# Kernel tuning notes

Hardware: AMD Instinct MI355X
Metric: run time of the kernel (lower is better)

## Reference

```python
import jax, jax.numpy as jnp
import numpy as np

B, F, H, T = 32, 128, 256, 2048


def setup_inputs() -> dict:
    key = jax.random.key(0)
    ks = jax.random.split(key, 20)
    s = 0.05
    x = jax.random.normal(ks[0], (B, 1, T, F), dtype=jnp.float32)
    mask = (jax.random.uniform(ks[1], (B, 1, T, F)) < 0.5).astype(jnp.float32)
    delta = jax.random.uniform(ks[2], (B, 1, T, F), dtype=jnp.float32)  # time since last obs
    inp = jnp.concatenate([x, mask, delta], axis=1)  # [B, 3, T, F]
    p = lambda k, shape: jax.random.normal(k, shape, dtype=jnp.float32) * s
    return {
        "input": inp,
        "x_mean": p(ks[3], (F,)),
        # layer 0: input decay (diagonal), hidden decay, gates
        "w_dx": p(ks[4], (F,)), "b_dx": p(ks[5], (F,)),
        "W_dh0": p(ks[6], (F, H)), "b_dh0": p(ks[7], (H,)),
        "W0": p(ks[8], (F, 3 * H)), "U0": p(ks[9], (H, 3 * H)),
        "V0": p(ks[10], (F, 3 * H)), "b0": p(ks[11], (3 * H,)),
        # layer 1: hidden decay from delta, gates (input = prev layer hidden)
        "W_dh1": p(ks[12], (F, H)), "b_dh1": p(ks[13], (H,)),
        "W1": p(ks[14], (H, 3 * H)), "U1": p(ks[15], (H, 3 * H)),
        "V1": p(ks[16], (F, 3 * H)), "b1": p(ks[17], (3 * H,)),
    }


def _grud_cell(x_in, m, delta, h, W_dh, b_dh, W, U, V, b):
    # hidden-state decay from delta-time
    gamma_h = jnp.exp(-jax.nn.relu(delta @ W_dh + b_dh))  # [B,H]
    h = gamma_h * h
    pre = x_in @ W + m @ V + b                             # [B,3H]
    hU = h @ U[:, : 2 * H]                                 # r,z recurrent terms
    r = jax.nn.sigmoid(pre[:, :H] + hU[:, :H])
    z = jax.nn.sigmoid(pre[:, H : 2 * H] + hU[:, H : 2 * H])
    h_tilde = jnp.tanh(pre[:, 2 * H :] + (r * h) @ U[:, 2 * H :])
    return (1.0 - z) * h + z * h_tilde


def reference(input, x_mean, w_dx, b_dx, W_dh0, b_dh0, W0, U0, V0, b0,
              W_dh1, b_dh1, W1, U1, V1, b1):
    xs = jnp.moveaxis(input, 2, 0)  # [T, B, 3, F]
    x_last0 = jnp.broadcast_to(x_mean, (B, F))
    h0 = jnp.zeros((B, H), dtype=input.dtype)
    h1 = jnp.zeros((B, H), dtype=input.dtype)

    def step(carry, inp_t):
        x_last, h0, h1 = carry
        x, m, delta = inp_t[:, 0], inp_t[:, 1], inp_t[:, 2]  # [B,F] each
        # input decay toward empirical mean (GRU-D imputation)
        gamma_x = jnp.exp(-jax.nn.relu(delta * w_dx + b_dx))
        x_hat = m * x + (1.0 - m) * (gamma_x * x_last + (1.0 - gamma_x) * x_mean)
        h0n = _grud_cell(x_hat, m, delta, h0, W_dh0, b_dh0, W0, U0, V0, b0)
        h1n = _grud_cell(h0n, m, delta, h1, W_dh1, b_dh1, W1, U1, V1, b1)
        x_last_new = jnp.where(m > 0, x, x_last)  # update AFTER the cells, as in torch
        return (x_last_new, h0n, h1n), h1n

    _, ys = jax.lax.scan(step, (x_last0, h0, h1), xs)
    return ys  # [T, B, H]
```

## Files before the change

### kernel.cpp

```cpp
#include <hip/hip_runtime.h>

typedef _Float16 f16;
typedef _Float16 f16x2 __attribute__((ext_vector_type(2)));
typedef unsigned int u32;

#define CB 32
#define CF 128
#define CH 256
#define CT 2048
#define TCC 64
#define SEG 16
#define SLEN 128
#define SHBYTES 16896
#define GBLK ((TCC*CB/64)*16/2)

static __device__ __forceinline__ f16x2 bc(u32 u){ return __builtin_bit_cast(f16x2, u); }
static __device__ __forceinline__ u32 packh2(float lo, float hi){ f16x2 v; v.x=(f16)lo; v.y=(f16)hi; return __builtin_bit_cast(u32, v); }

static __device__ __forceinline__ float dot2f(f16x2 a, f16x2 b, float c){
#if defined(__has_builtin)
#if __has_builtin(__builtin_amdgcn_fdot2)
  return __builtin_amdgcn_fdot2(a, b, c, false);
#else
  return c + (float)a.x*(float)b.x + (float)a.y*(float)b.y;
#endif
#else
  return c + (float)a.x*(float)b.x + (float)a.y*(float)b.y;
#endif
}
static __device__ __forceinline__ float dot4q(float acc, uint4 w, uint4 h){
  acc = dot2f(bc(w.x), bc(h.x), acc);
  acc = dot2f(bc(w.y), bc(h.y), acc);
  acc = dot2f(bc(w.z), bc(h.z), acc);
  acc = dot2f(bc(w.w), bc(h.w), acc);
  return acc;
}

template<int CTRL>
static __device__ __forceinline__ float dppx(float x){
  int v = __builtin_amdgcn_update_dpp(0, __builtin_bit_cast(int, x), CTRL, 0xF, 0xF, true);
  return x + __builtin_bit_cast(float, v);
}

#define PIN4(V) asm volatile("" : "+v"((V).x), "+v"((V).y), "+v"((V).z), "+v"((V).w))

#define RBAR() do { \
  asm volatile("s_waitcnt lgkmcnt(0)" ::: "memory"); \
  __builtin_amdgcn_s_barrier(); \
  asm volatile("" ::: "memory"); \
} while (0)

__global__ void init_hst(float* hst){
  int i = blockIdx.x*256 + threadIdx.x;
  if (i < 2*CB*CH) hst[i] = 0.f;
}

static __device__ __forceinline__ float wc0src(int k, int n, const float* W0, const float* V0, const float* Wdh0){
  if (k < 128) return (n < 768) ? W0[k*768 + n] : 0.f;
  if (k < 256) return (n < 768) ? V0[(k-128)*768 + n] : 0.f;
  return (n >= 768) ? Wdh0[(k-256)*256 + (n-768)] : 0.f;
}
static __device__ __forceinline__ float wc1src(int k, int n, const float* W1, const float* V1, const float* Wdh1){
  if (k < 256) return (n < 768) ? W1[k*768 + n] : 0.f;
  if (k < 384) return (n < 768) ? V1[(k-256)*768 + n] : 0.f;
  return (n >= 768) ? Wdh1[(k-384)*256 + (n-768)] : 0.f;
}
static __device__ __forceinline__ u32 wrz_pair(int flat, int jj, int L, const float* U){
  int p = L >> 2, q = L & 3;
  int cc = flat >> 3, j = flat & 7;
  int col = 4*p + cc;
  int pr = 32*q + 4*j + jj;
  return packh2(U[(2*pr)*768 + col], U[(2*pr+1)*768 + col]);
}
static __device__ __forceinline__ u32 wcc_pair(int flat, int jj, int L, const float* U){
  int p = L >> 2, q = L & 3;
  int cc2 = flat >> 3, j = flat & 7;
  int col = 512 + 2*p + cc2;
  int pr = 32*q + 4*j + jj;
  return packh2(U[(2*pr)*768 + col], U[(2*pr+1)*768 + col]);
}

__global__ __launch_bounds__(256) void pack_w(
    const float* __restrict__ W0, const float* __restrict__ V0, const float* __restrict__ Wdh0,
    const float* __restrict__ W1, const float* __restrict__ V1, const float* __restrict__ Wdh1,
    const float* __restrict__ U0, const float* __restrict__ U1,
    const float* __restrict__ b0, const float* __restrict__ bdh0,
    const float* __restrict__ b1, const float* __restrict__ bdh1,
    u32* __restrict__ WC0p, u32* __restrict__ WC1p,
    u32* __restrict__ WRZa, u32* __restrict__ WRZb,
    u32* __restrict__ WCCa, u32* __restrict__ WCCb,
    float* __restrict__ bias0, float* __restrict__ bias1){
  int idx = blockIdx.x*256 + threadIdx.x;
  if (idx < 196608){
    int k2 = idx >> 10, n = idx & 1023;
    WC0p[idx] = packh2(wc0src(2*k2, n, W0,V0,Wdh0), wc0src(2*k2+1, n, W0,V0,Wdh0));
  } else if (idx < 458752){
    int j = idx - 196608; int k2 = j >> 10, n = j & 1023;
    WC1p[j] = packh2(wc1src(2*k2, n, W1,V1,Wdh1), wc1src(2*k2+1, n, W1,V1,Wdh1));
  } else if (idx < 524288){
    int j = idx - 458752; int flat = j >> 11, L = (j >> 2) & 511, jj = j & 3;
    WRZa[j] = wrz_pair(flat, jj, L, U0);
  } else if (idx < 589824){
    int j = idx - 524288; int flat = j >> 11, L = (j >> 2) & 511, jj = j & 3;
    WRZb[j] = wrz_pair(flat, jj, L, U1);
  } else if (idx < 622592){
    int j = idx - 589824; int flat = j >> 11, L = (j >> 2) & 511, jj = j & 3;
    WCCa[j] = wcc_pair(flat, jj, L, U0);
  } else if (idx < 655360){
    int j = idx - 622592; int flat = j >> 11, L = (j >> 2) & 511, jj = j & 3;
    WCCb[j] = wcc_pair(flat, jj, L, U1);
  } else if (idx < 657408){
    int i = idx - 655360;
    if (i < 1024) bias0[i] = (i < 768) ? b0[i] : bdh0[i - 768];
    else { int j = i - 1024; bias1[j] = (j < 768) ? b1[j] : bdh1[j - 768]; }
  }
}

__global__ __launch_bounds__(256) void k1a(const float* __restrict__ in,
    float* __restrict__ segval, int* __restrict__ seghas){
  int tid = blockIdx.x*256 + threadIdx.x;
  int s = tid >> 12, chain = tid & 4095;
  int b = chain >> 7, f = chain & 127;
  const float* px = in + ((size_t)b*3 + 0)*CT*CF + f;
  const float* pm = in + ((size_t)b*3 + 1)*CT*CF + f;
  float last = 0.f; int has = 0;
  #pragma unroll 4
  for (int u = 0; u < SLEN; ++u){
    int t = s*SLEN + u;
    float m = pm[(size_t)t*CF], x = px[(size_t)t*CF];
    if (m > 0.f){ last = x; has = 1; }
  }
  segval[s*4096 + chain] = last;
  seghas[s*4096 + chain] = has;
}
__global__ __launch_bounds__(256) void k1b(const float* __restrict__ x_mean,
    const float* __restrict__ segval, const int* __restrict__ seghas, float* __restrict__ seed){
  int chain = blockIdx.x*256 + threadIdx.x;
  int f = chain & 127;
  float cur = x_mean[f];
  #pragma unroll
  for (int s = 0; s < SEG; ++s){
    seed[s*4096 + chain] = cur;
    if (seghas[s*4096 + chain]) cur = segval[s*4096 + chain];
  }
}
__global__ __launch_bounds__(256) void k1c(const float* __restrict__ in, const float* __restrict__ x_mean,
    const float* __restrict__ w_dx, const float* __restrict__ b_dx,
    const float* __restrict__ seed, f16* __restrict__ A){
  int tid = blockIdx.x*256 + threadIdx.x;
  int s = tid >> 12, chain = tid & 4095;
  int b = chain >> 7, f = chain & 127;
  const float wd = w_dx[f], bd = b_dx[f], xm = x_mean[f];
  const float* px = in + ((size_t)b*3 + 0)*CT*CF + f;
  const float* pm = in + ((size_t)b*3 + 1)*CT*CF + f;
  const float* pd = in + ((size_t)b*3 + 2)*CT*CF + f;
  float xl = seed[s*4096 + chain];
  #pragma unroll 4
  for (int u = 0; u < SLEN; ++u){
    int t = s*SLEN + u;
    float x = px[(size_t)t*CF], m = pm[(size_t)t*CF], d = pd[(size_t)t*CF];
    float gx = __expf(-fmaxf(d*wd + bd, 0.f));
    float xh = m*x + (1.f-m)*(gx*xl + (1.f-gx)*xm);
    f16* wq = A + ((size_t)t*CB + b)*384 + f;
    wq[0] = (f16)xh; wq[128] = (f16)m; wq[256] = (f16)d;
    xl = (m > 0.f) ? x : xl;
  }
}

static __device__ void gemm_tile(
    const u32* __restrict__ Aa, int lda, const u32* __restrict__ Ab, int ldb, int kasplit,
    int ktiles, const u32* __restrict__ Wp, const float* __restrict__ bias, float* __restrict__ Out,
    int row0, int n0, int tid, char* sm){
  u32 (*AsT)[68] = (u32 (*)[68])sm;
  u32 (*Bs)[64]  = (u32 (*)[64])(sm + 4352);
  const int tx = tid & 15, ty = tid >> 4;
  const int am = tid >> 2, akq = (tid & 3) * 4;
  const int bk = tid >> 4, bnq = (tid & 15) * 4;
  float acc[4][4] = {};
  for (int kt = 0; kt < ktiles; ++kt){
    int k2g = kt*16 + akq;
    uint4 ga;
    if (k2g < kasplit) ga = *(const uint4*)&Aa[(size_t)(row0 + am)*lda + k2g];
    else               ga = *(const uint4*)&Ab[(size_t)(row0 + am)*ldb + (k2g - kasplit)];
    uint4 gb = *(const uint4*)&Wp[(size_t)(kt*16 + bk)*1024 + n0 + bnq];
    __syncthreads();
    AsT[akq+0][am] = ga.x; AsT[akq+1][am] = ga.y; AsT[akq+2][am] = ga.z; AsT[akq+3][am] = ga.w;
    *(uint4*)&Bs[bk][bnq] = gb;
    __syncthreads();
    #pragma unroll
    for (int kk = 0; kk < 16; ++kk){
      uint4 bq = *(const uint4*)&Bs[kk][tx*4];
      uint4 aq = *(const uint4*)&AsT[kk][ty*4];
      f16x2 bv0 = bc(bq.x), bv1 = bc(bq.y), bv2 = bc(bq.z), bv3 = bc(bq.w);
      f16x2 av0 = bc(aq.x), av1 = bc(aq.y), av2 = bc(aq.z), av3 = bc(aq.w);
      acc[0][0] = dot2f(av0, bv0, acc[0][0]); acc[0][1] = dot2f(av0, bv1, acc[0][1]);
      acc[0][2] = dot2f(av0, bv2, acc[0][2]); acc[0][3] = dot2f(av0, bv3, acc[0][3]);
      acc[1][0] = dot2f(av1, bv0, acc[1][0]); acc[1][1] = dot2f(av1, bv1, acc[1][1]);
      acc[1][2] = dot2f(av1, bv2, acc[1][2]); acc[1][3] = dot2f(av1, bv3, acc[1][3]);
      acc[2][0] = dot2f(av2, bv0, acc[2][0]); acc[2][1] = dot2f(av2, bv1, acc[2][1]);
      acc[2][2] = dot2f(av2, bv2, acc[2][2]); acc[2][3] = dot2f(av2, bv3, acc[2][3]);
      acc[3][0] = dot2f(av3, bv0, acc[3][0]); acc[3][1] = dot2f(av3, bv1, acc[3][1]);
      acc[3][2] = dot2f(av3, bv2, acc[3][2]); acc[3][3] = dot2f(av3, bv3, acc[3][3]);
    }
  }
  const bool isg = (n0 >= 768);
  #pragma unroll
  for (int i = 0; i < 4; ++i){
    int r = row0 + ty*4 + i;
    int n = n0 + tx*4;
    float4 v;
    float* vv = (float*)&v;
    #pragma unroll
    for (int j = 0; j < 4; ++j){
      float x = acc[i][j] + bias[n + j];
      if (isg) x = __expf(-fmaxf(x, 0.f));
      vv[j] = x;
    }
    *(float4*)&Out[(size_t)r*1024 + n] = v;
  }
}

__global__ __launch_bounds__(512, 2) void mega(
    const float* __restrict__ O0r, const float* __restrict__ O1r,
    const u32* __restrict__ WRZa, const u32* __restrict__ WRZb,
    const u32* __restrict__ WCCa, const u32* __restrict__ WCCb,
    float* __restrict__ hst, f16* __restrict__ h0cw, float* __restrict__ out,
    int t0_l1, int n0, int n1, int g0n, int g1n,
    const u32* __restrict__ g0a, float* __restrict__ g0out,
    const u32* __restrict__ g1a, const u32* __restrict__ g1b, float* __restrict__ g1out,
    const u32* __restrict__ WC0p, const u32* __restrict__ WC1p,
    const float* __restrict__ bias0, const float* __restrict__ bias1){
  extern __shared__ __align__(16) char smraw[];
  const int L = threadIdx.x;
  if (blockIdx.x >= 64){
    int gb = blockIdx.x - 64;
    int st = L >> 8, t2 = L & 255;
    char* smst = smraw + st*8448;
    if (gb < g0n){
      int tile = gb*2 + st;
      gemm_tile(g0a, 192, g0a, 192, 192, 12, WC0p, bias0, g0out, (tile>>4)*64, (tile&15)*64, t2, smst);
    } else {
      int tile = (gb - g0n)*2 + st;
      gemm_tile(g1a, 128, g1b, 192, 128, 16, WC1p, bias1, g1out, (tile>>4)*64, (tile&15)*64, t2, smst);
    }
    return;
  }
  const int role = blockIdx.x >> 5;
  const int b = blockIdx.x & 31;
  const int steps = role ? n1 : n0;
  if (steps == 0) return;
  const float* O = role ? O1r : O0r;
  const u32* WRZ = role ? WRZb : WRZa;
  const u32* WCC = role ? WCCb : WCCa;
  float* hcarry = hst + role*CB*CH;

  f16*  hdh_  = (f16*)(smraw);
  f16*  rh_   = (f16*)(smraw + 640);
  float* hdf  = (float*)(smraw + 1280);
  float* zz   = (float*)(smraw + 2304);

  uint4 wrz[32];
  #pragma unroll
  for (int i = 0; i < 32; ++i) wrz[i] = *(const uint4*)&WRZ[((size_t)i*512 + L)*4];
  uint4 wcc[16];
  #pragma unroll
  for (int i = 0; i < 16; ++i) wcc[i] = *(const uint4*)&WCC[((size_t)i*512 + L)*4];
  #pragma unroll
  for (int i = 0; i < 32; ++i) PIN4(wrz[i]);
  #pragma unroll
  for (int i = 0; i < 16; ++i) PIN4(wcc[i]);

  __builtin_amdgcn_s_setprio(1);

  const int p = L >> 2, q = L & 3;
  size_t row = (size_t)b*1024;
  if (L < 256){
    float hd = O[row + 768 + L] * hcarry[b*256 + L];
    hdf[L] = hd; hdh_[(L>>6)*80 + (L&63)] = (f16)hd;
  }
  float prz = O[row + L];
  const int e2 = 2*p + (q & 1);
  float pc = (q < 2) ? O[row + 512 + e2] : 0.f;
  const char* hqb = (const char*)hdh_ + q*160;
  const char* rqb = (const char*)rh_ + q*160;
  __syncthreads();

  for (int lt = 0; lt < steps; ++lt){
    size_t nrow = row + (size_t)CB*1024;
    float nprz = 0.f, npc = 0.f, ngex = 0.f;
    if (lt + 1 < steps){
      nprz = O[nrow + L];
      if (q < 2){ npc = O[nrow + 512 + e2]; ngex = O[nrow + 768 + e2]; }
    }
    float hdL = (L < 256) ? hdf[L] : 0.f;
    float hd2 = hdf[e2];
    float a0=0.f, a1=0.f, a2=0.f, a3=0.f;
    #pragma unroll
    for (int j = 0; j < 8; ++j){
      uint4 h = ((const uint4*)hqb)[j];
      a0 = dot4q(a0, wrz[j],      h);
      a1 = dot4q(a1, wrz[8 + j],  h);
      a2 = dot4q(a2, wrz[16 + j], h);
      a3 = dot4q(a3, wrz[24 + j], h);
    }
    a0 = dppx<0xB1>(a0); a1 = dppx<0xB1>(a1); a2 = dppx<0xB1>(a2); a3 = dppx<0xB1>(a3);
    a0 = dppx<0x4E>(a0); a1 = dppx<0x4E>(a1); a2 = dppx<0x4E>(a2); a3 = dppx<0x4E>(a3);
    float sum1 = (q == 0) ? a0 : (q == 1) ? a1 : (q == 2) ? a2 : a3;
    float s1 = 1.f/(1.f + __expf(-(sum1 + prz)));
    if (L < 256) rh_[(L>>6)*80 + (L&63)] = (f16)(s1 * hdL);
    else zz[L - 256] = s1;
    RBAR();
    float z = zz[e2];
    float b0_=0.f, b1_=0.f;
    #pragma unroll
    for (int j = 0; j < 8; ++j){
      uint4 r = ((const uint4*)rqb)[j];
      b0_ = dot4q(b0_, wcc[j],     r);
      b1_ = dot4q(b1_, wcc[8 + j], r);
    }
    b0_ = dppx<0xB1>(b0_); b1_ = dppx<0xB1>(b1_);
    b0_ = dppx<0x4E>(b0_); b1_ = dppx<0x4E>(b1_);
    if (q < 2){
      float sumc = (q & 1) ? b1_ : b0_;
      float v = pc + sumc;
      float e = __expf(2.f*v);
      float ct = 1.f - 2.f/(1.f + e);
      float hd = hd2;
      float hn = hd + z*(ct - hd);
      float hdn = ngex*hn;
      hdf[e2] = hdn; hdh_[(e2>>6)*80 + (e2&63)] = (f16)hdn;
      if (role == 0) h0cw[((size_t)lt*CB + b)*256 + e2] = (f16)hn;
      else           out[((size_t)(t0_l1 + lt)*CB + b)*256 + e2] = hn;
      if (lt == steps-1) hcarry[b*256 + e2] = hn;
    }
    prz = nprz; pc = npc;
    row = nrow;
    RBAR();
  }
}

extern "C" void kernel_launch(void* const* d_in, const int* in_sizes, int n_in,
                              void* d_out, int out_size, void* d_ws, size_t ws_size,
                              hipStream_t stream){
  const float* input  = (const float*)d_in[0];
  const float* x_mean = (const float*)d_in[1];
  const float* w_dx   = (const float*)d_in[2];
  const float* b_dx   = (const float*)d_in[3];
  const float* Wdh0   = (const float*)d_in[4];
  const float* bdh0   = (const float*)d_in[5];
  const float* W0     = (const float*)d_in[6];
  const float* U0     = (const float*)d_in[7];
  const float* V0     = (const float*)d_in[8];
  const float* b0     = (const float*)d_in[9];
  const float* Wdh1   = (const float*)d_in[10];
  const float* bdh1   = (const float*)d_in[11];
  const float* W1     = (const float*)d_in[12];
  const float* U1     = (const float*)d_in[13];
  const float* V1     = (const float*)d_in[14];
  const float* b1     = (const float*)d_in[15];
  float* out = (float*)d_out;

  hipFuncSetAttribute((const void*)mega, hipFuncAttributeMaxDynamicSharedMemorySize, SHBYTES);

  char* base = (char*)d_ws;
  size_t off = 0;
  auto take = [&](size_t bytes)->char*{
    char* p = base + off;
    off = (off + bytes + 255) & ~(size_t)255;
    return p;
  };
  f16*  IN0h  = (f16*) take((size_t)CT*CB*384*2);
  u32*  WC0p  = (u32*) take((size_t)192*1024*4);
  u32*  WC1p  = (u32*) take((size_t)256*1024*4);
  u32*  WRZa  = (u32*) take((size_t)32*512*4*4);
  u32*  WRZb  = (u32*) take((size_t)32*512*4*4);
  u32*  WCCa  = (u32*) take((size_t)16*512*4*4);
  u32*  WCCb  = (u32*) take((size_t)16*512*4*4);
  float* bias0= (float*)take(1024*4);
  float* bias1= (float*)take(1024*4);
  float* hst  = (float*)take((size_t)2*CB*CH*4);
  float* segv = (float*)take((size_t)SEG*4096*4);
  int*   segh = (int*)  take((size_t)SEG*4096*4);
  float* seed = (float*)take((size_t)SEG*4096*4);
  float* O0b[2], *O1b[2]; f16* h0b[2];
  O0b[0] = (float*)take((size_t)TCC*CB*1024*4);
  O0b[1] = (float*)take((size_t)TCC*CB*1024*4);
  O1b[0] = (float*)take((size_t)TCC*CB*1024*4);
  O1b[1] = (float*)take((size_t)TCC*CB*1024*4);
  h0b[0] = (f16*)  take((size_t)TCC*CB*CH*2);
  h0b[1] = (f16*)  take((size_t)TCC*CB*CH*2);

  hipLaunchKernelGGL(init_hst, dim3(64), dim3(256), 0, stream, hst);
  hipLaunchKernelGGL(pack_w, dim3((657408 + 255)/256), dim3(256), 0, stream,
      W0, V0, Wdh0, W1, V1, Wdh1, U0, U1, b0, bdh0, b1, bdh1,
      WC0p, WC1p, WRZa, WRZb, WCCa, WCCb, bias0, bias1);
  hipLaunchKernelGGL(k1a, dim3(256), dim3(256), 0, stream, input, segv, segh);
  hipLaunchKernelGGL(k1b, dim3(16), dim3(256), 0, stream, x_mean, segv, segh, seed);
  hipLaunchKernelGGL(k1c, dim3(256), dim3(256), 0, stream, input, x_mean, w_dx, b_dx, seed, IN0h);

  const u32* IN0p = (const u32*)IN0h;
  const int nch = CT / TCC;
  for (int i = -1; i <= nch + 1; ++i){
    int r0 = (i >= 0 && i < nch) ? 1 : 0;
    int r1 = (i >= 2 && i < nch + 2) ? 1 : 0;
    int g0 = (i + 1 >= 0 && i + 1 < nch) ? 1 : 0;
    int g1 = (i - 1 >= 0 && i - 1 < nch) ? 1 : 0;
    int g0n = g0 ? GBLK : 0, g1n = g1 ? GBLK : 0;
    const float* O0r = O0b[i & 1];
    const float* O1r = O1b[i & 1];
    f16* h0cw = h0b[i & 1];
    const u32* g0a = IN0p + (size_t)(i+1)*TCC*CB*192;
    float* g0out = O0b[(i+1) & 1];
    const u32* g1a = (const u32*)h0b[(i-1) & 1];
    const u32* g1b = IN0p + (size_t)(i-1)*TCC*CB*192 + 64;
    float* g1out = O1b[(i-1) & 1];
    hipLaunchKernelGGL(mega, dim3(64 + g0n + g1n), dim3(512), SHBYTES, stream,
        O0r, O1r, WRZa, WRZb, WCCa, WCCb, hst, h0cw, out,
        (i-2)*TCC, r0 ? TCC : 0, r1 ? TCC : 0, g0n, g1n,
        g0a, g0out, g1a, g1b, g1out,
        WC0p, WC1p, bias0, bias1);
  }
}
```

Baseline: 3.161 ms.

## Replace per-chunk kernel launches with one persistent cooperative kernel using grid sync

The host loop that launched one mega kernel per time chunk becomes a single cooperative launch. Inside it, recurrent blocks and a fixed pool of 192 GEMM blocks iterate over the chunks and separate them with grid.sync. This removes per-launch overhead and the reload of the register-resident recurrent weights on every chunk. In exchange, the GEMM work is capped at 192 blocks, all 256 blocks must be co-resident for the cooperative launch to succeed, and each grid-wide barrier adds latency.

```diff
diff --git a/kernel.cpp b/kernel.cpp
--- a/kernel.cpp
+++ b/kernel.cpp
@@ -1,4 +1,7 @@
 #include <hip/hip_runtime.h>
+#include <hip/hip_cooperative_groups.h>
+
+namespace cg = cooperative_groups;
 
 typedef _Float16 f16;
 typedef _Float16 f16x2 __attribute__((ext_vector_type(2)));
@@ -12,7 +15,10 @@
 #define SEG 16
 #define SLEN 128
 #define SHBYTES 16896
-#define GBLK ((TCC*CB/64)*16/2)
+#define NGB 192
+#define NBLK (64 + NGB)
+#define NCH (CT / TCC)
+#define NSLOT ((TCC*CB/64)*16/2)
 
 static __device__ __forceinline__ f16x2 bc(u32 u){ return __builtin_bit_cast(f16x2, u); }
 static __device__ __forceinline__ u32 packh2(float lo, float hi){ f16x2 v; v.x=(f16)lo; v.y=(f16)hi; return __builtin_bit_cast(u32, v); }
@@ -220,36 +226,51 @@
   }
 }
 
-__global__ __launch_bounds__(512, 2) void mega(
-    const float* __restrict__ O0r, const float* __restrict__ O1r,
+__global__ __launch_bounds__(512, 2) void megap(
     const u32* __restrict__ WRZa, const u32* __restrict__ WRZb,
     const u32* __restrict__ WCCa, const u32* __restrict__ WCCb,
-    float* __restrict__ hst, f16* __restrict__ h0cw, float* __restrict__ out,
-    int t0_l1, int n0, int n1, int g0n, int g1n,
-    const u32* __restrict__ g0a, float* __restrict__ g0out,
-    const u32* __restrict__ g1a, const u32* __restrict__ g1b, float* __restrict__ g1out,
+    float* __restrict__ hst, float* __restrict__ out,
+    const u32* __restrict__ IN0p,
+    f16* __restrict__ h0b0, f16* __restrict__ h0b1,
+    float* __restrict__ O0b0, float* __restrict__ O0b1,
+    float* __restrict__ O1b0, float* __restrict__ O1b1,
     const u32* __restrict__ WC0p, const u32* __restrict__ WC1p,
     const float* __restrict__ bias0, const float* __restrict__ bias1){
+  cg::grid_group grid = cg::this_grid();
   extern __shared__ __align__(16) char smraw[];
   const int L = threadIdx.x;
+
   if (blockIdx.x >= 64){
-    int gb = blockIdx.x - 64;
-    int st = L >> 8, t2 = L & 255;
+    const int gw = blockIdx.x - 64;
+    const int st = L >> 8, t2 = L & 255;
     char* smst = smraw + st*8448;
-    if (gb < g0n){
-      int tile = gb*2 + st;
-      gemm_tile(g0a, 192, g0a, 192, 192, 12, WC0p, bias0, g0out, (tile>>4)*64, (tile&15)*64, t2, smst);
-    } else {
-      int tile = (gb - g0n)*2 + st;
-      gemm_tile(g1a, 128, g1b, 192, 128, 16, WC1p, bias1, g1out, (tile>>4)*64, (tile&15)*64, t2, smst);
+    for (int i = -1; i <= NCH + 1; ++i){
+      const bool g0 = (i+1 >= 0) && (i+1 < NCH);
+      const bool g1 = (i-1 >= 0) && (i-1 < NCH);
+      const u32* g0a = IN0p + (size_t)(i+1)*TCC*CB*192;
+      float* g0out = ((i+1) & 1) ? O0b1 : O0b0;
+      const u32* g1a = (const u32*)(((i-1) & 1) ? h0b1 : h0b0);
+      const u32* g1b = IN0p + (size_t)(i-1)*TCC*CB*192 + 64;
+      float* g1out = ((i-1) & 1) ? O1b1 : O1b0;
+      const int n0s = g0 ? NSLOT : 0;
+      const int tot = n0s + (g1 ? NSLOT : 0);
+      for (int slot = gw; slot < tot; slot += NGB){
+        if (slot < n0s){
+          int tile = slot*2 + st;
+          gemm_tile(g0a, 192, g0a, 192, 192, 12, WC0p, bias0, g0out, (tile>>4)*64, (tile&15)*64, t2, smst);
+        } else {
+          int tile = (slot - n0s)*2 + st;
+          gemm_tile(g1a, 128, g1b, 192, 128, 16, WC1p, bias1, g1out, (tile>>4)*64, (tile&15)*64, t2, smst);
+        }
+      }
+      __threadfence();
+      grid.sync();
+      __threadfence();
     }
     return;
   }
   const int role = blockIdx.x >> 5;
   const int b = blockIdx.x & 31;
-  const int steps = role ? n1 : n0;
-  if (steps == 0) return;
-  const float* O = role ? O1r : O0r;
   const u32* WRZ = role ? WRZb : WRZa;
   const u32* WCC = role ? WCCb : WCCa;
   float* hcarry = hst + role*CB*CH;
@@ -273,69 +294,81 @@
   __builtin_amdgcn_s_setprio(1);
 
   const int p = L >> 2, q = L & 3;
-  size_t row = (size_t)b*1024;
-  if (L < 256){
-    float hd = O[row + 768 + L] * hcarry[b*256 + L];
-    hdf[L] = hd; hdh_[(L>>6)*80 + (L&63)] = (f16)hd;
-  }
-  float prz = O[row + L];
   const int e2 = 2*p + (q & 1);
-  float pc = (q < 2) ? O[row + 512 + e2] : 0.f;
   const char* hqb = (const char*)hdh_ + q*160;
   const char* rqb = (const char*)rh_ + q*160;
-  __syncthreads();
-
-  for (int lt = 0; lt < steps; ++lt){
-    size_t nrow = row + (size_t)CB*1024;
-    float nprz = 0.f, npc = 0.f, ngex = 0.f;
-    if (lt + 1 < steps){
-      nprz = O[nrow + L];
-      if (q < 2){ npc = O[nrow + 512 + e2]; ngex = O[nrow + 768 + e2]; }
+
+  for (int i = -1; i <= NCH + 1; ++i){
+    const bool act = role ? (i >= 2 && i < NCH + 2) : (i >= 0 && i < NCH);
+    if (act){
+      const float* O = role ? ((i & 1) ? O1b1 : O1b0) : ((i & 1) ? O0b1 : O0b0);
+      f16* h0cw = (i & 1) ? h0b1 : h0b0;
+      const int t0_l1 = (i - 2)*TCC;
+      size_t row = (size_t)b*1024;
+      if (L < 256){
+        float hd = O[row + 768 + L] * hcarry[b*256 + L];
+        hdf[L] = hd; hdh_[(L>>6)*80 + (L&63)] = (f16)hd;
+      }
+      float prz = O[row + L];
+      float pc = (q < 2) ? O[row + 512 + e2] : 0.f;
+      __syncthreads();
+
+      for (int lt = 0; lt < TCC; ++lt){
+        size_t nrow = row + (size_t)CB*1024;
+        float nprz = 0.f, npc = 0.f, ngex = 0.f;
+        if (lt + 1 < TCC){
+          nprz = O[nrow + L];
+          if (q < 2){ npc = O[nrow + 512 + e2]; ngex = O[nrow + 768 + e2]; }
+        }
+        float hdL = (L < 256) ? hdf[L] : 0.f;
+        float hd2 = hdf[e2];
+        float a0=0.f, a1=0.f, a2=0.f, a3=0.f;
+        #pragma unroll
+        for (int j = 0; j < 8; ++j){
+          uint4 h = ((const uint4*)hqb)[j];
+          a0 = dot4q(a0, wrz[j],      h);
+          a1 = dot4q(a1, wrz[8 + j],  h);
+          a2 = dot4q(a2, wrz[16 + j], h);
+          a3 = dot4q(a3, wrz[24 + j], h);
+        }
+        a0 = dppx<0xB1>(a0); a1 = dppx<0xB1>(a1); a2 = dppx<0xB1>(a2); a3 = dppx<0xB1>(a3);
+        a0 = dppx<0x4E>(a0); a1 = dppx<0x4E>(a1); a2 = dppx<0x4E>(a2); a3 = dppx<0x4E>(a3);
+        float sum1 = (q == 0) ? a0 : (q == 1) ? a1 : (q == 2) ? a2 : a3;
+        float s1 = 1.f/(1.f + __expf(-(sum1 + prz)));
+        if (L < 256) rh_[(L>>6)*80 + (L&63)] = (f16)(s1 * hdL);
+        else zz[L - 256] = s1;
+        RBAR();
+        float z = zz[e2];
+        float b0_=0.f, b1_=0.f;
+        #pragma unroll
+        for (int j = 0; j < 8; ++j){
+          uint4 r = ((const uint4*)rqb)[j];
+          b0_ = dot4q(b0_, wcc[j],     r);
+          b1_ = dot4q(b1_, wcc[8 + j], r);
+        }
+        b0_ = dppx<0xB1>(b0_); b1_ = dppx<0xB1>(b1_);
+        b0_ = dppx<0x4E>(b0_); b1_ = dppx<0x4E>(b1_);
+        if (q < 2){
+          float sumc = (q & 1) ? b1_ : b0_;
+          float v = pc + sumc;
+          float e = __expf(2.f*v);
+          float ct = 1.f - 2.f/(1.f + e);
+          float hd = hd2;
+          float hn = hd + z*(ct - hd);
+          float hdn = ngex*hn;
+          hdf[e2] = hdn; hdh_[(e2>>6)*80 + (e2&63)] = (f16)hdn;
+          if (role == 0) h0cw[((size_t)lt*CB + b)*256 + e2] = (f16)hn;
+          else           out[((size_t)(t0_l1 + lt)*CB + b)*256 + e2] = hn;
+          if (lt == TCC-1) hcarry[b*256 + e2] = hn;
+        }
+        prz = nprz; pc = npc;
+        row = nrow;
+        RBAR();
+      }
     }
-    float hdL = (L < 256) ? hdf[L] : 0.f;
-    float hd2 = hdf[e2];
-    float a0=0.f, a1=0.f, a2=0.f, a3=0.f;
-    #pragma unroll
-    for (int j = 0; j < 8; ++j){
-      uint4 h = ((const uint4*)hqb)[j];
-      a0 = dot4q(a0, wrz[j],      h);
-      a1 = dot4q(a1, wrz[8 + j],  h);
-      a2 = dot4q(a2, wrz[16 + j], h);
-      a3 = dot4q(a3, wrz[24 + j], h);
-    }
-    a0 = dppx<0xB1>(a0); a1 = dppx<0xB1>(a1); a2 = dppx<0xB1>(a2); a3 = dppx<0xB1>(a3);
-    a0 = dppx<0x4E>(a0); a1 = dppx<0x4E>(a1); a2 = dppx<0x4E>(a2); a3 = dppx<0x4E>(a3);
-    float sum1 = (q == 0) ? a0 : (q == 1) ? a1 : (q == 2) ? a2 : a3;
-    float s1 = 1.f/(1.f + __expf(-(sum1 + prz)));
-    if (L < 256) rh_[(L>>6)*80 + (L&63)] = (f16)(s1 * hdL);
-    else zz[L - 256] = s1;
-    RBAR();
-    float z = zz[e2];
-    float b0_=0.f, b1_=0.f;
-    #pragma unroll
-    for (int j = 0; j < 8; ++j){
-      uint4 r = ((const uint4*)rqb)[j];
-      b0_ = dot4q(b0_, wcc[j],     r);
-      b1_ = dot4q(b1_, wcc[8 + j], r);
-    }
-    b0_ = dppx<0xB1>(b0_); b1_ = dppx<0xB1>(b1_);
-    b0_ = dppx<0x4E>(b0_); b1_ = dppx<0x4E>(b1_);
-    if (q < 2){
-      float sumc = (q & 1) ? b1_ : b0_;
-      float v = pc + sumc;
-      float e = __expf(2.f*v);
-      float ct = 1.f - 2.f/(1.f + e);
-      float hd = hd2;
-      float hn = hd + z*(ct - hd);
-      float hdn = ngex*hn;
-      hdf[e2] = hdn; hdh_[(e2>>6)*80 + (e2&63)] = (f16)hdn;
-      if (role == 0) h0cw[((size_t)lt*CB + b)*256 + e2] = (f16)hn;
-      else           out[((size_t)(t0_l1 + lt)*CB + b)*256 + e2] = hn;
-      if (lt == steps-1) hcarry[b*256 + e2] = hn;
-    }
-    prz = nprz; pc = npc;
-    row = nrow;
-    RBAR();
+    __threadfence();
+    grid.sync();
+    __threadfence();
   }
 }
 
@@ -360,7 +393,7 @@
   const float* b1     = (const float*)d_in[15];
   float* out = (float*)d_out;
 
-  hipFuncSetAttribute((const void*)mega, hipFuncAttributeMaxDynamicSharedMemorySize, SHBYTES);
+  hipFuncSetAttribute((const void*)megap, hipFuncAttributeMaxDynamicSharedMemorySize, SHBYTES);
 
   char* base = (char*)d_ws;
   size_t off = 0;
@@ -382,13 +415,12 @@
   float* segv = (float*)take((size_t)SEG*4096*4);
   int*   segh = (int*)  take((size_t)SEG*4096*4);
   float* seed = (float*)take((size_t)SEG*4096*4);
-  float* O0b[2], *O1b[2]; f16* h0b[2];
-  O0b[0] = (float*)take((size_t)TCC*CB*1024*4);
-  O0b[1] = (float*)take((size_t)TCC*CB*1024*4);
-  O1b[0] = (float*)take((size_t)TCC*CB*1024*4);
-  O1b[1] = (float*)take((size_t)TCC*CB*1024*4);
-  h0b[0] = (f16*)  take((size_t)TCC*CB*CH*2);
-  h0b[1] = (f16*)  take((size_t)TCC*CB*CH*2);
+  float* O0b0 = (float*)take((size_t)TCC*CB*1024*4);
+  float* O0b1 = (float*)take((size_t)TCC*CB*1024*4);
+  float* O1b0 = (float*)take((size_t)TCC*CB*1024*4);
+  float* O1b1 = (float*)take((size_t)TCC*CB*1024*4);
+  f16*  h0b0  = (f16*)  take((size_t)TCC*CB*CH*2);
+  f16*  h0b1  = (f16*)  take((size_t)TCC*CB*CH*2);
 
   hipLaunchKernelGGL(init_hst, dim3(64), dim3(256), 0, stream, hst);
   hipLaunchKernelGGL(pack_w, dim3((657408 + 255)/256), dim3(256), 0, stream,
@@ -399,25 +431,12 @@
   hipLaunchKernelGGL(k1c, dim3(256), dim3(256), 0, stream, input, x_mean, w_dx, b_dx, seed, IN0h);
 
   const u32* IN0p = (const u32*)IN0h;
-  const int nch = CT / TCC;
-  for (int i = -1; i <= nch + 1; ++i){
-    int r0 = (i >= 0 && i < nch) ? 1 : 0;
-    int r1 = (i >= 2 && i < nch + 2) ? 1 : 0;
-    int g0 = (i + 1 >= 0 && i + 1 < nch) ? 1 : 0;
-    int g1 = (i - 1 >= 0 && i - 1 < nch) ? 1 : 0;
-    int g0n = g0 ? GBLK : 0, g1n = g1 ? GBLK : 0;
-    const float* O0r = O0b[i & 1];
-    const float* O1r = O1b[i & 1];
-    f16* h0cw = h0b[i & 1];
-    const u32* g0a = IN0p + (size_t)(i+1)*TCC*CB*192;
-    float* g0out = O0b[(i+1) & 1];
-    const u32* g1a = (const u32*)h0b[(i-1) & 1];
-    const u32* g1b = IN0p + (size_t)(i-1)*TCC*CB*192 + 64;
-    float* g1out = O1b[(i-1) & 1];
-    hipLaunchKernelGGL(mega, dim3(64 + g0n + g1n), dim3(512), SHBYTES, stream,
-        O0r, O1r, WRZa, WRZb, WCCa, WCCb, hst, h0cw, out,
-        (i-2)*TCC, r0 ? TCC : 0, r1 ? TCC : 0, g0n, g1n,
-        g0a, g0out, g1a, g1b, g1out,
-        WC0p, WC1p, bias0, bias1);
-  }
-}
+  void* args[] = {
+    (void*)&WRZa, (void*)&WRZb, (void*)&WCCa, (void*)&WCCb,
+    (void*)&hst, (void*)&out, (void*)&IN0p,
+    (void*)&h0b0, (void*)&h0b1,
+    (void*)&O0b0, (void*)&O0b1, (void*)&O1b0, (void*)&O1b1,
+    (void*)&WC0p, (void*)&WC1p, (void*)&bias0, (void*)&bias1
+  };
+  hipLaunchCooperativeKernel((const void*)megap, dim3(NBLK), dim3(512), args, SHBYTES, stream);
+}
```

Measured after the change: 5.984 ms. 89.3% more time.
